# Performance work log

Hardware: AMD Instinct MI355X
Metric: run time of the kernel (lower is better)

The kernel has to match this reference:

```python
import jax, jax.numpy as jnp
import numpy as np

D_MODEL = 1024
NHEAD = 16
HEAD_DIM = D_MODEL // NHEAD
DFF = 4096
EPS = 1e-5


def _layernorm(x, g, b):
    mu = jnp.mean(x, axis=-1, keepdims=True)
    var = jnp.mean(jnp.square(x - mu), axis=-1, keepdims=True)
    return (x - mu) * jax.lax.rsqrt(var + EPS) * g + b


def setup_inputs() -> dict:
    key = jax.random.key(0)
    ks = jax.random.split(key, 20)
    B, S = 2, 2048
    s = 0.02
    inp = {
        "src": jax.random.normal(ks[0], (B, S, D_MODEL), jnp.float32),
        "recompute_idx": jnp.sort(jax.random.randint(ks[1], (409,), 0, S)),
        "cached_k": jax.random.normal(ks[2], (B, NHEAD, S, HEAD_DIM), jnp.float32),
        "cached_v": jax.random.normal(ks[3], (B, NHEAD, S, HEAD_DIM), jnp.float32),
        "Wq": jax.random.normal(ks[4], (D_MODEL, D_MODEL), jnp.float32) * s,
        "bq": jnp.zeros((D_MODEL,), jnp.float32),
        "Wk": jax.random.normal(ks[5], (D_MODEL, D_MODEL), jnp.float32) * s,
        "bk": jnp.zeros((D_MODEL,), jnp.float32),
        "Wv": jax.random.normal(ks[6], (D_MODEL, D_MODEL), jnp.float32) * s,
        "bv": jnp.zeros((D_MODEL,), jnp.float32),
        "Wo": jax.random.normal(ks[7], (D_MODEL, D_MODEL), jnp.float32) * s,
        "bo": jnp.zeros((D_MODEL,), jnp.float32),
        "W1": jax.random.normal(ks[8], (DFF, D_MODEL), jnp.float32) * s,
        "b1": jnp.zeros((DFF,), jnp.float32),
        "W2": jax.random.normal(ks[9], (D_MODEL, DFF), jnp.float32) * s,
        "b2": jnp.zeros((D_MODEL,), jnp.float32),
        "g1": jnp.ones((D_MODEL,), jnp.float32),
        "beta1": jnp.zeros((D_MODEL,), jnp.float32),
        "g2": jnp.ones((D_MODEL,), jnp.float32),
        "beta2": jnp.zeros((D_MODEL,), jnp.float32),
    }
    return inp


def reference(src, recompute_idx, cached_k, cached_v, Wq, bq, Wk, bk, Wv, bv,
              Wo, bo, W1, b1, W2, b2, g1, beta1, g2, beta2):
    B, S, D = src.shape
    H, hd = NHEAD, HEAD_DIM

    # Q for all tokens
    q = (src @ Wq.T + bq).reshape(B, S, H, hd).transpose(0, 2, 1, 3)  # [B,H,S,hd]

    # K/V recomputed only for selected tokens, scattered over cached KV
    src_rec = src[:, recompute_idx, :]  # [B,R,D]
    R = src_rec.shape[1]
    k_rec = (src_rec @ Wk.T + bk).reshape(B, R, H, hd).transpose(0, 2, 1, 3)
    v_rec = (src_rec @ Wv.T + bv).reshape(B, R, H, hd).transpose(0, 2, 1, 3)
    k_full = cached_k.at[:, :, recompute_idx, :].set(k_rec)  # [B,H,S,hd]
    v_full = cached_v.at[:, :, recompute_idx, :].set(v_rec)

    # attention over mixed cached/fresh KV
    scores = jnp.einsum('bhqd,bhkd->bhqk', q, k_full) / np.sqrt(hd).astype(src.dtype)
    probs = jax.nn.softmax(scores, axis=-1)
    attn = jnp.einsum('bhqk,bhkd->bhqd', probs, v_full)
    attn = attn.transpose(0, 2, 1, 3).reshape(B, S, D)
    attn = attn @ Wo.T + bo

    x = _layernorm(src + attn, g1, beta1)
    ff = jax.nn.relu(x @ W1.T + b1) @ W2.T + b2
    x = _layernorm(x + ff, g2, beta2)
    return x
```

## Files before the change

kernel.cpp:

```cpp
#include <hip/hip_runtime.h>
#include <hip/hip_bf16.h>

typedef __attribute__((ext_vector_type(4))) float f32x4;
typedef __attribute__((ext_vector_type(8))) short s16x8;
typedef __attribute__((ext_vector_type(4))) short s16x4;
typedef __attribute__((ext_vector_type(2))) short s16x2;

typedef __attribute__((address_space(1))) const unsigned int guint;
typedef __attribute__((address_space(3))) unsigned int luint;

#define D_MODEL 1024
#define NHEAD 16
#define HEAD_DIM 64
#define DFF 4096
#define SEQ 2048
#define BATCH 2
#define QSCALE 0.18033688011112042f

__device__ __forceinline__ float b2f(short s) {
  union { unsigned int u; float f; } v;
  v.u = ((unsigned int)(unsigned short)s) << 16;
  return v.f;
}
__device__ __forceinline__ short f2b(float f) {
  __hip_bfloat16 h = __float2bfloat16(f);
  return *reinterpret_cast<short*>(&h);
}
__device__ __forceinline__ s16x8 cvt8(f32x4 a, f32x4 b) {
  s16x8 r;
  #pragma unroll
  for (int i = 0; i < 4; ++i) { r[i] = f2b(a[i]); r[i + 4] = f2b(b[i]); }
  return r;
}

template<int MODE, int BN, bool AF32, bool WF32>
__global__ __launch_bounds__(256, 3)
void gemm_nt(const void* __restrict__ Av, const void* __restrict__ Wv,
             const float* __restrict__ bias, short* __restrict__ out,
             int M, int N, int K,
             const int* __restrict__ idx, int R,
             const float* __restrict__ bias2, const float* __restrict__ bias3,
             short* __restrict__ pB, short* __restrict__ pC,
             short* __restrict__ pD)
{
  constexpr bool GLDS = (!AF32 && !WF32);
  constexpr int NI = BN / 32;

  const float* Af = (const float*)Av;
  const short* Ab = (const short*)Av;
  const float* Wf = (const float*)Wv;
  const short* Wb = (const short*)Wv;

  const int tid  = threadIdx.x;
  const int lane = tid & 63, wave = tid >> 6;
  const int g = lane >> 4, l15 = lane & 15;
  const int wm = (wave & 1) * 64, wn = (wave >> 1) * (BN / 2);

  const int nwg = gridDim.x * gridDim.y;
  int lid = blockIdx.y * gridDim.x + blockIdx.x;
  if ((nwg & 7) == 0) lid = (lid & 7) * (nwg >> 3) + (lid >> 3);
  const int bn = lid % gridDim.x;
  const int bm0 = lid / gridDim.x;

  int task = 0, bm = bm0, Mt = M;
  if (MODE == 8) {
    if (bm0 < 32)      { task = 0; bm = bm0;      Mt = M; }
    else if (bm0 < 39) { task = 1; bm = bm0 - 32; Mt = BATCH * R; }
    else               { task = 2; bm = bm0 - 39; Mt = BATCH * R; }
  }

  f32x4 acc[4][NI] = {};

  if constexpr (GLDS) {
    __shared__ short As[2][128][32];
    __shared__ short Bs[2][BN][32];

    const short* Wbase = Wb + ((MODE == 8) ? ((size_t)task << 20) : 0);
    const int nz   = (MODE == 6) ? gridDim.z : 1;
    const int Keff = K / nz;
    const int kOff = (MODE == 6) ? (int)blockIdx.z * Keff : 0;

    const int rA0 = wave * 16 + (lane >> 2);
    const int rA1 = rA0 + 64;
    const int cs = (((lane & 3) ^ ((lane >> 3) & 3)) * 8);

    auto arow = [&](int r) -> long {
      const int gm = bm * 128 + r;
      const int am = gm < Mt ? gm : Mt - 1;
      if (MODE == 8 && task > 0) {
        const int b0 = am / R;
        return (long)(b0 * SEQ + idx[am - b0 * R]);
      }
      return am;
    };
    const long aR0 = arow(rA0), aR1 = arow(rA1);
    const long wR0 = (long)bn * BN + rA0;

    const short* gA0 = Ab + aR0 * K + kOff + cs;
    const short* gA1 = Ab + aR1 * K + kOff + cs;
    const short* gB0 = Wbase + wR0 * K + kOff + cs;
    const short* gB1 = nullptr;
    if constexpr (BN == 128) gB1 = Wbase + ((long)bn * BN + rA1) * K + kOff + cs;

    auto stage = [&](int buf, int k0) {
      luint* lA0 = (luint*)((short*)As + buf * 4096 + wave * 512);
      luint* lA1 = (luint*)((short*)As + buf * 4096 + (4 + wave) * 512);
      luint* lB0 = (luint*)((short*)Bs + buf * (BN * 32) + wave * 512);
      __builtin_amdgcn_global_load_lds((guint*)(gA0 + k0), lA0, 16, 0, 0);
      __builtin_amdgcn_global_load_lds((guint*)(gA1 + k0), lA1, 16, 0, 0);
      __builtin_amdgcn_global_load_lds((guint*)(gB0 + k0), lB0, 16, 0, 0);
      if constexpr (BN == 128) {
        luint* lB1 = (luint*)((short*)Bs + buf * (BN * 32) + (4 + wave) * 512);
        __builtin_amdgcn_global_load_lds((guint*)(gB1 + k0), lB1, 16, 0, 0);
      }
    };

    const int rcol = ((g ^ ((l15 >> 1) & 3)) * 8);

    const int nt = Keff / 32;
    stage(0, 0);
    int cur = 0;
    for (int t = 0; t < nt; ++t) {
      if (t + 1 < nt) {
        stage(cur ^ 1, (t + 1) * 32);
        if constexpr (BN == 128) asm volatile("s_waitcnt vmcnt(4)" ::: "memory");
        else                     asm volatile("s_waitcnt vmcnt(3)" ::: "memory");
      } else {
        asm volatile("s_waitcnt vmcnt(0)" ::: "memory");
      }
      __builtin_amdgcn_s_barrier();
      __builtin_amdgcn_sched_barrier(0);

      s16x8 af[4], bf4[NI];
      #pragma unroll
      for (int mi = 0; mi < 4; ++mi)
        af[mi] = *(const s16x8*)&As[cur][wm + mi * 16 + l15][rcol];
      #pragma unroll
      for (int ni = 0; ni < NI; ++ni)
        bf4[ni] = *(const s16x8*)&Bs[cur][wn + ni * 16 + l15][rcol];
      #pragma unroll
      for (int mi = 0; mi < 4; ++mi)
        #pragma unroll
        for (int ni = 0; ni < NI; ++ni)
          acc[mi][ni] = __builtin_amdgcn_mfma_f32_16x16x32_bf16(af[mi], bf4[ni], acc[mi][ni], 0, 0, 0);

      __builtin_amdgcn_sched_barrier(0);
      __builtin_amdgcn_s_barrier();
      cur ^= 1;
    }
  } else {
    __shared__ short As[128][40];
    __shared__ short Bs[128][40];
    const int r0 = tid >> 1, c0 = (tid & 1) * 16;
    const int gm0 = bm * 128 + r0;
    const int am0 = gm0 < M ? gm0 : M - 1;
    long aRow0;
    if (MODE == 3 || MODE == 4) {
      const int b0 = am0 / R;
      aRow0 = (long)(b0 * SEQ + idx[am0 - b0 * R]);
    } else {
      aRow0 = am0;
    }
    const long wRow0 = bn * 128 + r0;

    for (int k0 = 0; k0 < K; k0 += 32) {
      __syncthreads();
      if (AF32) {
        f32x4 a0 = *(const f32x4*)(Af + aRow0 * K + k0 + c0);
        f32x4 a1 = *(const f32x4*)(Af + aRow0 * K + k0 + c0 + 4);
        f32x4 a2 = *(const f32x4*)(Af + aRow0 * K + k0 + c0 + 8);
        f32x4 a3 = *(const f32x4*)(Af + aRow0 * K + k0 + c0 + 12);
        *(s16x8*)&As[r0][c0]     = cvt8(a0, a1);
        *(s16x8*)&As[r0][c0 + 8] = cvt8(a2, a3);
      } else {
        *(s16x8*)&As[r0][c0]     = *(const s16x8*)(Ab + aRow0 * K + k0 + c0);
        *(s16x8*)&As[r0][c0 + 8] = *(const s16x8*)(Ab + aRow0 * K + k0 + c0 + 8);
      }
      if (WF32) {
        f32x4 w0 = *(const f32x4*)(Wf + wRow0 * K + k0 + c0);
        f32x4 w1 = *(const f32x4*)(Wf + wRow0 * K + k0 + c0 + 4);
        f32x4 w2 = *(const f32x4*)(Wf + wRow0 * K + k0 + c0 + 8);
        f32x4 w3 = *(const f32x4*)(Wf + wRow0 * K + k0 + c0 + 12);
        *(s16x8*)&Bs[r0][c0]     = cvt8(w0, w1);
        *(s16x8*)&Bs[r0][c0 + 8] = cvt8(w2, w3);
      } else {
        *(s16x8*)&Bs[r0][c0]     = *(const s16x8*)(Wb + wRow0 * K + k0 + c0);
        *(s16x8*)&Bs[r0][c0 + 8] = *(const s16x8*)(Wb + wRow0 * K + k0 + c0 + 8);
      }
      __syncthreads();

      s16x8 af[4], bf4[4];
      #pragma unroll
      for (int mi = 0; mi < 4; ++mi)
        af[mi] = *(const s16x8*)&As[wm + mi * 16 + l15][g * 8];
      #pragma unroll
      for (int ni = 0; ni < 4; ++ni)
        bf4[ni] = *(const s16x8*)&Bs[wn + ni * 16 + l15][g * 8];
      #pragma unroll
      for (int mi = 0; mi < 4; ++mi)
        #pragma unroll
        for (int ni = 0; ni < 4; ++ni)
          acc[mi][ni % NI] = __builtin_amdgcn_mfma_f32_16x16x32_bf16(af[mi], bf4[ni], acc[mi][ni % NI], 0, 0, 0);
    }
  }

  short* outz = out;
  if (MODE == 6) {
    const int z = blockIdx.z;
    outz = (z == 0) ? out : (z == 1) ? pB : (z == 2) ? pC : pD;
  }

  #pragma unroll
  for (int mi = 0; mi < 4; ++mi) {
    #pragma unroll
    for (int ni = 0; ni < NI; ++ni) {
      const int gn = bn * BN + wn + ni * 16 + l15;
      float bv;
      if (MODE == 6)      bv = 0.f;
      else if (MODE == 8) bv = (task == 0) ? bias[gn] : (task == 1) ? bias2[gn] : bias3[gn];
      else                bv = bias[gn];
      #pragma unroll
      for (int r = 0; r < 4; ++r) {
        const int gm = bm * 128 + wm + mi * 16 + g * 4 + r;
        if (MODE == 8) { if (gm >= Mt) continue; }
        else           { if (gm >= M)  continue; }
        float v = acc[mi][ni][r] + bv;
        if (MODE == 1) v = v > 0.f ? v : 0.f;
        if (MODE == 2) v *= QSCALE;
        if (MODE == 0 || MODE == 1) {
          out[(long)gm * N + gn] = f2b(v);
        } else if (MODE == 2) {
          const int b = gm >> 11, s = gm & (SEQ - 1);
          const int h = gn >> 6, d = gn & 63;
          out[(((long)(b * NHEAD + h)) * SEQ + s) * 64 + d] = f2b(v);
        } else if (MODE == 3) {
          const int b = gm / R, s = idx[gm - b * R];
          const int h = gn >> 6, d = gn & 63;
          out[(((long)(b * NHEAD + h)) * SEQ + s) * 64 + d] = f2b(v);
        } else if (MODE == 4) {
          const int b = gm / R, s = idx[gm - b * R];
          const int h = gn >> 6, d = gn & 63;
          out[(((long)(b * NHEAD + h)) * 64 + d) * SEQ + s] = f2b(v);
        } else if (MODE == 6) {
          outz[(long)gm * N + gn] = f2b(v);
        } else {
          const int h = gn >> 6, d = gn & 63;
          if (task == 0) {
            const int b = gm >> 11, s = gm & (SEQ - 1);
            out[(((long)(b * NHEAD + h)) * SEQ + s) * 64 + d] = f2b(v * QSCALE);
          } else if (task == 1) {
            const int b = gm / R, s = idx[gm - b * R];
            (out + (1L << 22))[(((long)(b * NHEAD + h)) * SEQ + s) * 64 + d] = f2b(v);
          } else {
            const int b = gm / R, s = idx[gm - b * R];
            (out + (1L << 23))[(((long)(b * NHEAD + h)) * 64 + d) * SEQ + s] = f2b(v);
          }
        }
      }
    }
  }
}

__global__ __launch_bounds__(256, 2)
void attn_fwd(const short* __restrict__ Q, const short* __restrict__ Kf,
              const short* __restrict__ Vt, short* __restrict__ out)
{
  __shared__ short Kl[2][64][64];
  __shared__ short Vl[2][64][64];

  const int tid  = threadIdx.x;
  const int lane = tid & 63, w = tid >> 6;
  const int g = lane >> 4, l15 = lane & 15;
  const int bh = blockIdx.x;
  const int qt = blockIdx.y;
  const int b  = bh >> 4, h = bh & 15;

  const long base = (long)bh * SEQ * 64;
  const int  q0   = qt * 128 + w * 32;

  s16x8 qf[2][2];
  #pragma unroll
  for (int mi = 0; mi < 2; ++mi)
    #pragma unroll
    for (int c = 0; c < 2; ++c)
      qf[mi][c] = *(const s16x8*)(Q + base + (long)(q0 + mi * 16 + l15) * 64 + c * 32 + g * 8);

  f32x4 o[2][4] = {};
  f32x4 os[2] = {};

  s16x8 ones;
  #pragma unroll
  for (int j = 0; j < 8; ++j) ones[j] = (short)0x3F80;

  auto ldsw = [](short (*buf)[64], int row, int slot) -> short* {
    return (short*)((char*)&buf[0][0] + row * 128 + ((slot ^ (row & 7)) << 4));
  };

  const int bo0 = w * 2048 + lane * 16;
  const int bo1 = bo0 + 1024;
  const int row0 = bo0 >> 7, ss0 = (((bo0 >> 4) & 7) ^ (row0 & 7));
  const int row1 = bo1 >> 7, ss1 = (((bo1 >> 4) & 7) ^ (row1 & 7));
  const short* gK0 = Kf + base + row0 * 64 + ss0 * 8;
  const short* gK1 = Kf + base + row1 * 64 + ss1 * 8;
  const short* gV0 = Vt + base + (long)row0 * SEQ + ss0 * 8;
  const short* gV1 = Vt + base + (long)row1 * SEQ + ss1 * 8;

  auto stage = [&](int buf, int t) {
    char* kb8 = (char*)&Kl[buf][0][0] + w * 2048;
    char* vb8 = (char*)&Vl[buf][0][0] + w * 2048;
    __builtin_amdgcn_global_load_lds((guint*)(gK0 + t * 4096), (luint*)kb8, 16, 0, 0);
    __builtin_amdgcn_global_load_lds((guint*)(gK1 + t * 4096), (luint*)(kb8 + 1024), 16, 0, 0);
    __builtin_amdgcn_global_load_lds((guint*)(gV0 + t * 64), (luint*)vb8, 16, 0, 0);
    __builtin_amdgcn_global_load_lds((guint*)(gV1 + t * 64), (luint*)(vb8 + 1024), 16, 0, 0);
  };

  stage(0, 0);
  int cur = 0;
  for (int t = 0; t < SEQ / 64; ++t) {
    if (t + 1 < SEQ / 64) {
      stage(cur ^ 1, t + 1);
      asm volatile("s_waitcnt vmcnt(4)" ::: "memory");
    } else {
      asm volatile("s_waitcnt vmcnt(0)" ::: "memory");
    }
    __builtin_amdgcn_s_barrier();
    __builtin_amdgcn_sched_barrier(0);

    f32x4 sc[2][4] = {};
    __builtin_amdgcn_s_setprio(1);
    #pragma unroll
    for (int c = 0; c < 2; ++c)
      #pragma unroll
      for (int n = 0; n < 4; ++n) {
        s16x8 kb = *(const s16x8*)ldsw(Kl[cur], n * 16 + l15, c * 4 + g);
        sc[0][n] = __builtin_amdgcn_mfma_f32_16x16x32_bf16(kb, qf[0][c], sc[0][n], 0, 0, 0);
        sc[1][n] = __builtin_amdgcn_mfma_f32_16x16x32_bf16(kb, qf[1][c], sc[1][n], 0, 0, 0);
      }
    __builtin_amdgcn_s_setprio(0);

    s16x8 pa[2][2];
    #pragma unroll
    for (int mi = 0; mi < 2; ++mi) {
      #pragma unroll
      for (int n = 0; n < 4; ++n)
        #pragma unroll
        for (int r = 0; r < 4; ++r) {
          float e;
          asm("v_exp_f32 %0, %1" : "=v"(e) : "v"(sc[mi][n][r]));
          sc[mi][n][r] = e;
        }
      unsigned int wpk[4][2];
      #pragma unroll
      for (int n = 0; n < 4; ++n)
        #pragma unroll
        for (int p = 0; p < 2; ++p)
          asm("v_cvt_pk_bf16_f32 %0, %1, %2"
              : "=v"(wpk[n][p]) : "v"(sc[mi][n][2 * p]), "v"(sc[mi][n][2 * p + 1]));
      #pragma unroll
      for (int c = 0; c < 2; ++c) {
        union { s16x8 v; unsigned int u[4]; } pu;
        #pragma unroll
        for (int p = 0; p < 2; ++p) {
          unsigned int a = wpk[2 * c][p], bb = wpk[2 * c + 1][p];
          asm volatile("v_permlane32_swap_b32 %0, %1" : "+v"(a), "+v"(bb));
          asm volatile("v_permlane16_swap_b32 %0, %1" : "+v"(a), "+v"(bb));
          pu.u[p]     = a;
          pu.u[2 + p] = bb;
        }
        pa[mi][c] = pu.v;
      }
    }

    __builtin_amdgcn_s_setprio(1);
    #pragma unroll
    for (int dt = 0; dt < 4; ++dt)
      #pragma unroll
      for (int c = 0; c < 2; ++c) {
        s16x8 vb = *(const s16x8*)ldsw(Vl[cur], dt * 16 + l15, c * 4 + g);
        o[0][dt] = __builtin_amdgcn_mfma_f32_16x16x32_bf16(pa[0][c], vb, o[0][dt], 0, 0, 0);
        o[1][dt] = __builtin_amdgcn_mfma_f32_16x16x32_bf16(pa[1][c], vb, o[1][dt], 0, 0, 0);
      }
    #pragma unroll
    for (int mi = 0; mi < 2; ++mi)
      #pragma unroll
      for (int c = 0; c < 2; ++c)
        os[mi] = __builtin_amdgcn_mfma_f32_16x16x32_bf16(pa[mi][c], ones, os[mi], 0, 0, 0);
    __builtin_amdgcn_s_setprio(0);

    __builtin_amdgcn_sched_barrier(0);
    __builtin_amdgcn_s_barrier();
    cur ^= 1;
  }

  float inv[2][4];
  #pragma unroll
  for (int mi = 0; mi < 2; ++mi)
    #pragma unroll
    for (int r = 0; r < 4; ++r)
      inv[mi][r] = 1.0f / os[mi][r];

  #pragma unroll
  for (int mi = 0; mi < 2; ++mi)
    #pragma unroll
    for (int dt = 0; dt < 4; ++dt)
      #pragma unroll
      for (int r = 0; r < 4; ++r) {
        const int q   = q0 + mi * 16 + g * 4 + r;
        const int col = h * 64 + dt * 16 + l15;
        out[((long)(b * SEQ + q)) * D_MODEL + col] = f2b(o[mi][dt][r] * inv[mi][r]);
      }
}

template<bool RES_F32, bool OUT_F32>
__global__ __launch_bounds__(256, 4)
void ln_ff2(const short* __restrict__ p0, const short* __restrict__ p1,
            const float* __restrict__ bias, const void* __restrict__ resv,
            const float* __restrict__ g, const float* __restrict__ beta,
            void* __restrict__ outv)
{
  __shared__ float red[8];
  const int row = blockIdx.x;
  const int tid = threadIdx.x;
  const int lane = tid & 63, w = tid >> 6;

  s16x4 v0 = *(const s16x4*)(p0 + (long)row * D_MODEL + tid * 4);
  s16x4 v1 = *(const s16x4*)(p1 + (long)row * D_MODEL + tid * 4);
  f32x4 vb = *(const f32x4*)(bias + tid * 4);
  float x[4];
  if (RES_F32) {
    f32x4 vr = *(const f32x4*)((const float*)resv + (long)row * D_MODEL + tid * 4);
    #pragma unroll
    for (int i = 0; i < 4; ++i) x[i] = vr[i] + b2f(v0[i]) + b2f(v1[i]) + vb[i];
  } else {
    s16x4 vr = *(const s16x4*)((const short*)resv + (long)row * D_MODEL + tid * 4);
    #pragma unroll
    for (int i = 0; i < 4; ++i) x[i] = b2f(vr[i]) + b2f(v0[i]) + b2f(v1[i]) + vb[i];
  }

  float sum = x[0] + x[1] + x[2] + x[3];
  #pragma unroll
  for (int msk = 32; msk >= 1; msk >>= 1) sum += __shfl_xor(sum, msk, 64);
  if (lane == 0) red[w] = sum;
  __syncthreads();
  sum = red[0] + red[1] + red[2] + red[3];
  const float mu = sum * (1.f / D_MODEL);

  float sq = 0.f;
  #pragma unroll
  for (int i = 0; i < 4; ++i) { float d = x[i] - mu; sq += d * d; }
  #pragma unroll
  for (int msk = 32; msk >= 1; msk >>= 1) sq += __shfl_xor(sq, msk, 64);
  if (lane == 0) red[4 + w] = sq;
  __syncthreads();
  sq = red[4] + red[5] + red[6] + red[7];
  const float rs = rsqrtf(sq * (1.f / D_MODEL) + 1e-5f);

  if (OUT_F32) {
    f32x4 ov;
    #pragma unroll
    for (int i = 0; i < 4; ++i) {
      const int c = tid * 4 + i;
      ov[i] = (x[i] - mu) * rs * g[c] + beta[c];
    }
    *(f32x4*)((float*)outv + (long)row * D_MODEL + tid * 4) = ov;
  } else {
    s16x4 ov;
    #pragma unroll
    for (int i = 0; i < 4; ++i) {
      const int c = tid * 4 + i;
      ov[i] = f2b((x[i] - mu) * rs * g[c] + beta[c]);
    }
    *(s16x4*)((short*)outv + (long)row * D_MODEL + tid * 4) = ov;
  }
}

__global__ __launch_bounds__(256, 4)
void ln_ff4(const short* __restrict__ p0, const short* __restrict__ p1,
            const short* __restrict__ p2, const short* __restrict__ p3,
            const float* __restrict__ bias, const short* __restrict__ xres,
            const float* __restrict__ g, const float* __restrict__ beta,
            float* __restrict__ outv)
{
  __shared__ float red[8];
  const int row = blockIdx.x;
  const int tid = threadIdx.x;
  const int lane = tid & 63, w = tid >> 6;

  s16x4 v0 = *(const s16x4*)(p0 + (long)row * D_MODEL + tid * 4);
  s16x4 v1 = *(const s16x4*)(p1 + (long)row * D_MODEL + tid * 4);
  s16x4 v2 = *(const s16x4*)(p2 + (long)row * D_MODEL + tid * 4);
  s16x4 v3 = *(const s16x4*)(p3 + (long)row * D_MODEL + tid * 4);
  s16x4 vx = *(const s16x4*)(xres + (long)row * D_MODEL + tid * 4);
  f32x4 vb = *(const f32x4*)(bias + tid * 4);
  float x[4];
  #pragma unroll
  for (int i = 0; i < 4; ++i)
    x[i] = b2f(vx[i]) + b2f(v0[i]) + b2f(v1[i]) + b2f(v2[i]) + b2f(v3[i]) + vb[i];

  float sum = x[0] + x[1] + x[2] + x[3];
  #pragma unroll
  for (int msk = 32; msk >= 1; msk >>= 1) sum += __shfl_xor(sum, msk, 64);
  if (lane == 0) red[w] = sum;
  __syncthreads();
  sum = red[0] + red[1] + red[2] + red[3];
  const float mu = sum * (1.f / D_MODEL);

  float sq = 0.f;
  #pragma unroll
  for (int i = 0; i < 4; ++i) { float d = x[i] - mu; sq += d * d; }
  #pragma unroll
  for (int msk = 32; msk >= 1; msk >>= 1) sq += __shfl_xor(sq, msk, 64);
  if (lane == 0) red[4 + w] = sq;
  __syncthreads();
  sq = red[4] + red[5] + red[6] + red[7];
  const float rs = rsqrtf(sq * (1.f / D_MODEL) + 1e-5f);

  f32x4 ov;
  #pragma unroll
  for (int i = 0; i < 4; ++i) {
    const int c = tid * 4 + i;
    ov[i] = (x[i] - mu) * rs * g[c] + beta[c];
  }
  *(f32x4*)(outv + (long)row * D_MODEL + tid * 4) = ov;
}

template<bool RES_F32, bool OUT_F32>
__global__ __launch_bounds__(256, 4)
void ln_res(const short* __restrict__ a, const void* __restrict__ resv,
            const float* __restrict__ g, const float* __restrict__ beta,
            void* __restrict__ outv)
{
  __shared__ float red[8];
  const int row = blockIdx.x;
  const int tid = threadIdx.x;
  const int lane = tid & 63, w = tid >> 6;

  s16x4 va = *(const s16x4*)(a + (long)row * D_MODEL + tid * 4);
  float x[4];
  if (RES_F32) {
    f32x4 vr = *(const f32x4*)((const float*)resv + (long)row * D_MODEL + tid * 4);
    #pragma unroll
    for (int i = 0; i < 4; ++i) x[i] = b2f(va[i]) + vr[i];
  } else {
    s16x4 vr = *(const s16x4*)((const short*)resv + (long)row * D_MODEL + tid * 4);
    #pragma unroll
    for (int i = 0; i < 4; ++i) x[i] = b2f(va[i]) + b2f(vr[i]);
  }
  float sum = x[0] + x[1] + x[2] + x[3];
  #pragma unroll
  for (int msk = 32; msk >= 1; msk >>= 1) sum += __shfl_xor(sum, msk, 64);
  if (lane == 0) red[w] = sum;
  __syncthreads();
  sum = red[0] + red[1] + red[2] + red[3];
  const float mu = sum * (1.f / D_MODEL);

  float sq = 0.f;
  #pragma unroll
  for (int i = 0; i < 4; ++i) { float d = x[i] - mu; sq += d * d; }
  #pragma unroll
  for (int msk = 32; msk >= 1; msk >>= 1) sq += __shfl_xor(sq, msk, 64);
  if (lane == 0) red[4 + w] = sq;
  __syncthreads();
  sq = red[4] + red[5] + red[6] + red[7];
  const float rs = rsqrtf(sq * (1.f / D_MODEL) + 1e-5f);

  if (OUT_F32) {
    f32x4 ov;
    #pragma unroll
    for (int i = 0; i < 4; ++i) {
      const int c = tid * 4 + i;
      ov[i] = (x[i] - mu) * rs * g[c] + beta[c];
    }
    *(f32x4*)((float*)outv + (long)row * D_MODEL + tid * 4) = ov;
  } else {
    s16x4 ov;
    #pragma unroll
    for (int i = 0; i < 4; ++i) {
      const int c = tid * 4 + i;
      ov[i] = f2b((x[i] - mu) * rs * g[c] + beta[c]);
    }
    *(s16x4*)((short*)outv + (long)row * D_MODEL + tid * 4) = ov;
  }
}

__global__ void cvt_all(const float* __restrict__ ck, const float* __restrict__ cv,
                        const float* __restrict__ src,
                        const float* __restrict__ Wq, const float* __restrict__ Wk,
                        const float* __restrict__ Wv, const float* __restrict__ Wo,
                        const float* __restrict__ W1, const float* __restrict__ W2,
                        short* __restrict__ k_ws, short* __restrict__ v_ws,
                        short* __restrict__ srcb,
                        short* __restrict__ Wqb, short* __restrict__ W1b,
                        short* __restrict__ W2b)
{
  for (int i = blockIdx.x * blockDim.x + threadIdx.x; i < 5767168;
       i += gridDim.x * blockDim.x) {
    if (i >= 5242880) {
      const int j = i - 5242880;
      const int bh = j >> 14;
      const int rem = j & 16383;
      const int d = rem & 63;
      const int s0 = (rem >> 6) << 3;
      s16x8 r;
      #pragma unroll
      for (int k = 0; k < 8; ++k)
        r[k] = f2b(cv[((long)bh * SEQ + s0 + k) * 64 + d]);
      *(s16x8*)(v_ws + ((long)bh * 64 + d) * SEQ + s0) = r;
      continue;
    }
    const float* s; short* d; int li;
    if      (i < 1048576) { s = ck;  d = k_ws;           li = i; }
    else if (i < 2097152) { s = src; d = srcb;           li = i - 1048576; }
    else if (i < 2359296) { s = Wq;  d = Wqb;            li = i - 2097152; }
    else if (i < 2621440) { s = Wk;  d = Wqb + 1048576;  li = i - 2359296; }
    else if (i < 2883584) { s = Wv;  d = Wqb + 2097152;  li = i - 2621440; }
    else if (i < 3145728) { s = Wo;  d = Wqb + 3145728;  li = i - 2883584; }
    else if (i < 4194304) { s = W1;  d = W1b;            li = i - 3145728; }
    else                  { s = W2;  d = W2b;            li = i - 4194304; }
    f32x4 v = *(const f32x4*)(s + (long)li * 4);
    s16x4 r;
    #pragma unroll
    for (int j = 0; j < 4; ++j) r[j] = f2b(v[j]);
    *(s16x4*)(d + (long)li * 4) = r;
  }
}

__global__ void cvt_v_t(const float* __restrict__ in, short* __restrict__ out)
{
  const int c2 = blockIdx.x * blockDim.x + threadIdx.x;
  const int bh = c2 >> 14;
  const int rem = c2 & 16383;
  const int d = rem & 63;
  const int s0 = (rem >> 6) << 3;
  s16x8 r;
  #pragma unroll
  for (int j = 0; j < 8; ++j)
    r[j] = f2b(in[((long)bh * SEQ + s0 + j) * 64 + d]);
  *(s16x8*)(out + ((long)bh * 64 + d) * SEQ + s0) = r;
}

__global__ void cvt_f32_bf16(const f32x4* __restrict__ in, s16x4* __restrict__ out, int n4)
{
  for (int i = blockIdx.x * blockDim.x + threadIdx.x; i < n4; i += gridDim.x * blockDim.x) {
    f32x4 v = in[i];
    s16x4 r;
    #pragma unroll
    for (int j = 0; j < 4; ++j) r[j] = f2b(v[j]);
    out[i] = r;
  }
}

extern "C" void kernel_launch(void* const* d_in, const int* in_sizes, int n_in,
                              void* d_out, int out_size, void* d_ws, size_t ws_size,
                              hipStream_t stream)
{
  const float* src = (const float*)d_in[0];
  const int*   idx = (const int*)  d_in[1];
  const float* ck  = (const float*)d_in[2];
  const float* cv  = (const float*)d_in[3];
  const float* Wq  = (const float*)d_in[4];
  const float* bq  = (const float*)d_in[5];
  const float* Wk  = (const float*)d_in[6];
  const float* bk  = (const float*)d_in[7];
  const float* Wv  = (const float*)d_in[8];
  const float* bv  = (const float*)d_in[9];
  const float* Wo  = (const float*)d_in[10];
  const float* bo  = (const float*)d_in[11];
  const float* W1  = (const float*)d_in[12];
  const float* b1  = (const float*)d_in[13];
  const float* W2  = (const float*)d_in[14];
  const float* b2  = (const float*)d_in[15];
  const float* g1  = (const float*)d_in[16];
  const float* be1 = (const float*)d_in[17];
  const float* g2  = (const float*)d_in[18];
  const float* be2 = (const float*)d_in[19];
  float* out = (float*)d_out;

  char* ws = (char*)d_ws;
  const size_t SZ = (size_t)4096 * 1024 * 2;
  short* x_ws    = (short*)(ws);
  short* proj_ws = (short*)(ws + SZ);
  short* q_ws    = (short*)(ws + 2 * SZ);
  short* k_ws    = (short*)(ws + 3 * SZ);
  short* v_ws    = (short*)(ws + 4 * SZ);
  short* attn_ws = (short*)(ws + 5 * SZ);
  short* h_ws    = (short*)(ws + 2 * SZ);
  short* W1b     = (short*)(ws + 6 * SZ);
  short* W2b     = (short*)(ws + 7 * SZ);
  short* srcb    = (short*)(ws + 8 * SZ);
  short* Wqb     = (short*)(ws + 9 * SZ);
  const bool big = ws_size >= 10 * SZ;

  const int M = BATCH * SEQ;
  const int R = 409;
  const int Mr = BATCH * R;
  const int nkv4 = BATCH * NHEAD * SEQ * HEAD_DIM / 4;

  if (big) {
    cvt_all<<<2048, 256, 0, stream>>>(ck, cv, src, Wq, Wk, Wv, Wo, W1, W2,
                                      k_ws, v_ws, srcb, Wqb, W1b, W2b);
    gemm_nt<8, 64, false, false><<<dim3(16, 46), 256, 0, stream>>>(
        srcb, Wqb, bq, q_ws, M, 1024, 1024, idx, R, bk, bv, nullptr, nullptr, nullptr);
    attn_fwd<<<dim3(BATCH * NHEAD, SEQ / 128), 256, 0, stream>>>(q_ws, k_ws, v_ws, attn_ws);
    gemm_nt<6, 64, false, false><<<dim3(16, 32, 2), 256, 0, stream>>>(
        attn_ws, Wqb + 3145728, nullptr, proj_ws, M, 1024, 1024, nullptr, 0,
        nullptr, nullptr, q_ws, nullptr, nullptr);
    ln_ff2<true, false><<<4096, 256, 0, stream>>>(proj_ws, q_ws, bo, src, g1, be1, x_ws);
    gemm_nt<1, 128, false, false><<<dim3(32, 32), 256, 0, stream>>>(
        x_ws, W1b, b1, h_ws, M, DFF, 1024, nullptr, 0, nullptr, nullptr,
        nullptr, nullptr, nullptr);
    gemm_nt<6, 128, false, false><<<dim3(8, 32, 4), 256, 0, stream>>>(
        h_ws, W2b, nullptr, proj_ws, M, 1024, 4096, nullptr, 0,
        nullptr, nullptr, W1b, srcb, Wqb);
    ln_ff4<<<4096, 256, 0, stream>>>(proj_ws, W1b, srcb, Wqb, b2, x_ws, g2, be2, out);
  } else {
    cvt_f32_bf16<<<2048, 256, 0, stream>>>((const f32x4*)ck, (s16x4*)k_ws, nkv4);
    cvt_v_t<<<2048, 256, 0, stream>>>(cv, v_ws);
    gemm_nt<2, 128, true, true><<<dim3(8, 32), 256, 0, stream>>>(
        src, Wq, bq, q_ws, M, 1024, 1024, nullptr, 0, nullptr, nullptr, nullptr, nullptr, nullptr);
    gemm_nt<3, 128, true, true><<<dim3(8, 7), 256, 0, stream>>>(
        src, Wk, bk, k_ws, Mr, 1024, 1024, idx, R, nullptr, nullptr, nullptr, nullptr, nullptr);
    gemm_nt<4, 128, true, true><<<dim3(8, 7), 256, 0, stream>>>(
        src, Wv, bv, v_ws, Mr, 1024, 1024, idx, R, nullptr, nullptr, nullptr, nullptr, nullptr);
    attn_fwd<<<dim3(BATCH * NHEAD, SEQ / 128), 256, 0, stream>>>(q_ws, k_ws, v_ws, attn_ws);
    gemm_nt<0, 128, false, true><<<dim3(8, 32), 256, 0, stream>>>(
        attn_ws, Wo, bo, proj_ws, M, 1024, 1024, nullptr, 0, nullptr, nullptr, nullptr, nullptr, nullptr);
    ln_res<true, false><<<4096, 256, 0, stream>>>(proj_ws, src, g1, be1, x_ws);
    gemm_nt<1, 128, false, true><<<dim3(32, 32), 256, 0, stream>>>(
        x_ws, W1, b1, h_ws, M, DFF, 1024, nullptr, 0, nullptr, nullptr, nullptr, nullptr, nullptr);
    gemm_nt<0, 128, false, true><<<dim3(8, 32), 256, 0, stream>>>(
        h_ws, W2, b2, proj_ws, M, 1024, DFF, nullptr, 0, nullptr, nullptr, nullptr, nullptr, nullptr);
    ln_res<false, true><<<4096, 256, 0, stream>>>(proj_ws, x_ws, g2, be2, out);
  }
}
```

Before: 238.9 us.

## Add 256x256-tile 8-wave bf16 GEMM kernel for feed-forward layers

Adds a new GEMM kernel with 256x256 output tiles, 512 threads (8 waves), double-buffered LDS staging via global_load_lds with an XOR swizzle, and interleaved prefetch during the MFMA phases. It replaces the two feed-forward GEMMs (W1 with bias+ReLU, and the split-K W2). The larger tiles raise arithmetic intensity and cut global and LDS traffic per FLOP, and the workgroup ID remap aims to improve L2 locality. In exchange it needs 128KB of LDS and heavy register use, which limits occupancy, and the W1 grid shrinks to 256 blocks.

```diff
diff --git a/kernel.cpp b/kernel.cpp
--- a/kernel.cpp
+++ b/kernel.cpp
@@ -31,6 +31,130 @@
   #pragma unroll
   for (int i = 0; i < 4; ++i) { r[i] = f2b(a[i]); r[i + 4] = f2b(b[i]); }
   return r;
+}
+
+template<int MODE>
+__global__ __launch_bounds__(512, 2)
+void gemm_ff8(const short* __restrict__ A, const short* __restrict__ W,
+              const float* __restrict__ bias, short* __restrict__ out,
+              int N, int K,
+              short* __restrict__ pB, short* __restrict__ pC,
+              short* __restrict__ pD)
+{
+  __shared__ short Al[2][16384];
+  __shared__ short Bl[2][16384];
+
+  const int tid  = threadIdx.x;
+  const int lane = tid & 63, wave = tid >> 6;
+  const int g = lane >> 4, l15 = lane & 15;
+  const int wm = (wave >> 2) * 128;
+  const int wn = (wave & 3) * 64;
+
+  const int nwg = gridDim.x * gridDim.y;
+  int lid = blockIdx.y * gridDim.x + blockIdx.x;
+  if ((nwg & 7) == 0) lid = (lid & 7) * (nwg >> 3) + (lid >> 3);
+  const int bn = lid % gridDim.x, bm = lid / gridDim.x;
+
+  const int Keff = (MODE == 1) ? (K >> 2) : K;
+  const int kOff = (MODE == 1) ? (int)blockIdx.z * Keff : 0;
+
+  const int srow = tid >> 3;
+  const int scol = ((tid & 7) * 8) ^ (((tid >> 5) & 3) << 3);
+  const short* gA = A + ((long)(bm * 256) + srow) * K + kOff + scol;
+  const short* gW = W + ((long)(bn * 256) + srow) * K + kOff + scol;
+  const long slotG = 64L * K;
+
+  auto stage = [&](int buf, int slot, int k0) {
+    luint* dA = (luint*)((short*)Al + buf * 16384 + slot * 4096 + wave * 512);
+    luint* dB = (luint*)((short*)Bl + buf * 16384 + slot * 4096 + wave * 512);
+    __builtin_amdgcn_global_load_lds((guint*)(gA + slot * slotG + k0), dA, 16, 0, 0);
+    __builtin_amdgcn_global_load_lds((guint*)(gW + slot * slotG + k0), dB, 16, 0, 0);
+  };
+
+  const int rcbase = (g * 8) ^ ((l15 >> 2) << 3);
+
+  f32x4 acc[8][4] = {};
+
+  #pragma unroll
+  for (int s = 0; s < 4; ++s) stage(0, s, 0);
+
+  const int nt = Keff / 64;
+  int cur = 0;
+  for (int t = 0; t < nt; ++t) {
+    const int k1 = (t + 1) * 64;
+    if (t + 1 < nt) {
+      stage(cur ^ 1, 0, k1);
+      asm volatile("s_waitcnt vmcnt(2)" ::: "memory");
+    } else {
+      asm volatile("s_waitcnt vmcnt(0)" ::: "memory");
+    }
+    __builtin_amdgcn_s_barrier();
+    __builtin_amdgcn_sched_barrier(0);
+
+    const short* Abuf = (const short*)Al + cur * 16384;
+    const short* Bbuf = (const short*)Bl + cur * 16384;
+
+    #pragma unroll
+    for (int p = 0; p < 4; ++p) {
+      if (p > 0 && t + 1 < nt) stage(cur ^ 1, p, k1);
+      const int mq = p >> 1, nq = p & 1;
+
+      s16x8 av[4][2], bv2[2][2];
+      #pragma unroll
+      for (int mi = 0; mi < 4; ++mi) {
+        const int row = wm + (mq * 4 + mi) * 16 + l15;
+        #pragma unroll
+        for (int kk = 0; kk < 2; ++kk)
+          av[mi][kk] = *(const s16x8*)(Abuf + row * 64 + kk * 32 + rcbase);
+      }
+      #pragma unroll
+      for (int ni = 0; ni < 2; ++ni) {
+        const int row = wn + (nq * 2 + ni) * 16 + l15;
+        #pragma unroll
+        for (int kk = 0; kk < 2; ++kk)
+          bv2[ni][kk] = *(const s16x8*)(Bbuf + row * 64 + kk * 32 + rcbase);
+      }
+      asm volatile("s_waitcnt lgkmcnt(0)" ::: "memory");
+      __builtin_amdgcn_sched_barrier(0);
+
+      __builtin_amdgcn_s_setprio(1);
+      #pragma unroll
+      for (int mi = 0; mi < 4; ++mi)
+        #pragma unroll
+        for (int ni = 0; ni < 2; ++ni)
+          #pragma unroll
+          for (int kk = 0; kk < 2; ++kk)
+            acc[mq * 4 + mi][nq * 2 + ni] =
+                __builtin_amdgcn_mfma_f32_16x16x32_bf16(
+                    av[mi][kk], bv2[ni][kk], acc[mq * 4 + mi][nq * 2 + ni], 0, 0, 0);
+      __builtin_amdgcn_s_setprio(0);
+    }
+
+    __builtin_amdgcn_sched_barrier(0);
+    __builtin_amdgcn_s_barrier();
+    cur ^= 1;
+  }
+
+  short* oz = out;
+  if (MODE == 1) {
+    const int z = blockIdx.z;
+    oz = (z == 0) ? out : (z == 1) ? pB : (z == 2) ? pC : pD;
+  }
+  #pragma unroll
+  for (int MI = 0; MI < 8; ++MI) {
+    #pragma unroll
+    for (int NI2 = 0; NI2 < 4; ++NI2) {
+      const int gn = bn * 256 + wn + NI2 * 16 + l15;
+      const float bv = (MODE == 0) ? bias[gn] : 0.f;
+      #pragma unroll
+      for (int r = 0; r < 4; ++r) {
+        const int gm = bm * 256 + wm + MI * 16 + g * 4 + r;
+        float v = acc[MI][NI2][r] + bv;
+        if (MODE == 0) v = v > 0.f ? v : 0.f;
+        oz[(long)gm * N + gn] = f2b(v);
+      }
+    }
+  }
 }
 
 template<int MODE, int BN, bool AF32, bool WF32>
@@ -706,12 +830,10 @@
         attn_ws, Wqb + 3145728, nullptr, proj_ws, M, 1024, 1024, nullptr, 0,
         nullptr, nullptr, q_ws, nullptr, nullptr);
     ln_ff2<true, false><<<4096, 256, 0, stream>>>(proj_ws, q_ws, bo, src, g1, be1, x_ws);
-    gemm_nt<1, 128, false, false><<<dim3(32, 32), 256, 0, stream>>>(
-        x_ws, W1b, b1, h_ws, M, DFF, 1024, nullptr, 0, nullptr, nullptr,
-        nullptr, nullptr, nullptr);
-    gemm_nt<6, 128, false, false><<<dim3(8, 32, 4), 256, 0, stream>>>(
-        h_ws, W2b, nullptr, proj_ws, M, 1024, 4096, nullptr, 0,
-        nullptr, nullptr, W1b, srcb, Wqb);
+    gemm_ff8<0><<<dim3(16, 16), 512, 0, stream>>>(
+        x_ws, W1b, b1, h_ws, DFF, 1024, nullptr, nullptr, nullptr);
+    gemm_ff8<1><<<dim3(4, 16, 4), 512, 0, stream>>>(
+        h_ws, W2b, nullptr, proj_ws, 1024, 4096, W1b, srcb, Wqb);
     ln_ff4<<<4096, 256, 0, stream>>>(proj_ws, W1b, srcb, Wqb, b2, x_ws, g2, be2, out);
   } else {
     cvt_f32_bf16<<<2048, 256, 0, stream>>>((const f32x4*)ck, (s16x4*)k_ws, nkv4);
```

New measurement: 266.7 us. 11.6% more time.
